# Optimization experiments

Hardware: AMD Instinct MI355X
Metric: run time of the kernel (lower is better)

Reference implementation:

```python
import jax, jax.numpy as jnp
import numpy as np
import math

B, D, S, C, H = 8192, 512, 5, 2048, 4

def setup_inputs() -> dict:
    key = jax.random.key(0)
    ks = jax.random.split(key, 8)
    return {
        "features": jax.random.normal(ks[0], (B, D), dtype=jnp.float32),
        "logits": jax.random.normal(ks[1], (S, B, C), dtype=jnp.float32),
        "scale_feats": jax.random.normal(ks[2], (S, B, D), dtype=jnp.float32),
        "Wq": jax.random.normal(ks[3], (D, D), dtype=jnp.float32) * 0.02,
        "bq": jnp.zeros((D,), jnp.float32),
        "Wk": jax.random.normal(ks[4], (D, D), dtype=jnp.float32) * 0.02,
        "bk": jnp.zeros((D,), jnp.float32),
        "Wv": jax.random.normal(ks[5], (D, D), dtype=jnp.float32) * 0.02,
        "bv": jnp.zeros((D,), jnp.float32),
        "scale_emb": jax.random.normal(ks[6], (S, D), dtype=jnp.float32) * 0.02,
        "temperature": jnp.float32(0.07),
        "attn_w": jnp.ones((3,), jnp.float32) / 3.0,
    }

def reference(features, logits, scale_feats, Wq, bq, Wk, bk, Wv, bv, scale_emb, temperature, attn_w):
    b, d = features.shape
    s = scale_feats.shape[0]
    hd = d // H
    t = jnp.abs(temperature)

    # ---- multihead attention over scales (V is computed in torch but unused) ----
    Q = (features @ Wq + bq).reshape(b, H, hd)                      # [B,H,hd]
    sf_emb = scale_feats + scale_emb[:, None, :]                    # [S,B,D]
    K = (sf_emb @ Wk + bk).reshape(s, b, H, hd)                     # [S,B,H,hd]
    scores = jnp.einsum('bhd,sbhd->bhs', Q, K) / jnp.float32(math.sqrt(hd))
    attn_mha = jax.nn.softmax(scores / t, axis=-1).mean(axis=1)     # [B,S]

    # ---- geometric (angular) attention ----
    fn = features / jnp.linalg.norm(features, axis=-1, keepdims=True).clip(1e-12)
    sfn = scale_feats / jnp.linalg.norm(scale_feats, axis=-1, keepdims=True).clip(1e-12)
    cos_sim = jnp.einsum('bd,sbd->bs', fn, sfn)                     # [B,S]
    angles = jnp.arccos(jnp.clip(cos_sim, -1.0 + 1e-7, 1.0 - 1e-7))
    attn_geo = jax.nn.softmax(jnp.exp(-angles / t), axis=-1)        # [B,S]

    # ---- Cayley-Menger volume-proxy attention ----
    # simplex points: [features, scale_feat, cos(a)*f + sin(a)*s for a in {pi/4, pi/2, 3pi/4}]
    c = jnp.float32(math.sqrt(0.5))
    cf = jnp.array([1.0, 0.0, c, 0.0, -c], jnp.float32)             # coeffs on features
    cs = jnp.array([0.0, 1.0, c, 1.0, c], jnp.float32)              # coeffs on scale_feat
    simplex = (cf[None, :, None, None] * features[None, None] +
               cs[None, :, None, None] * scale_feats[:, None])      # [S,5,B,D]
    norms = jnp.sum(simplex * simplex, axis=-1)                     # [S,5,B]
    gram = jnp.einsum('spbd,sqbd->spqb', simplex, simplex)          # [S,5,5,B]
    distsq = norms[:, :, None] + norms[:, None, :] - 2.0 * gram     # [S,5,5,B]
    volumes = distsq.mean(axis=(1, 2)).T                            # [B,S]
    attn_cay = jax.nn.softmax(volumes / t, axis=-1)

    # ---- fuse attention types ----
    w = jax.nn.softmax(attn_w, axis=0)
    combined = w[0] * attn_mha + w[1] * attn_geo + w[2] * attn_cay  # [B,S]
    combined = combined / combined.sum(axis=-1, keepdims=True)

    combined_logits = jnp.einsum('bs,sbc->bc', combined, logits)    # [B,C]
    return (combined_logits, combined)
```

## Files before the change

kernel.cpp:

```cpp
#include <hip/hip_runtime.h>
#include <math.h>

#define B_N 8192
#define D_N 512
#define S_N 5
#define C_N 2048
#define H_N 4

typedef __attribute__((ext_vector_type(8))) short bf16x8;
typedef __attribute__((ext_vector_type(4))) float floatx4;

__device__ __forceinline__ float bf2f(short u) {
  union { unsigned int i; float f; } c;
  c.i = ((unsigned int)(unsigned short)u) << 16;
  return c.f;
}
__device__ __forceinline__ short f2bf(float f) {
  union { float f; unsigned int i; } c; c.f = f;
  unsigned int x = c.i;
  x += 0x7fffu + ((x >> 16) & 1u);
  return (short)(x >> 16);
}
__device__ __forceinline__ unsigned long long pack4(float a, float b, float c, float d) {
  return (unsigned long long)(unsigned short)f2bf(a)
       | ((unsigned long long)(unsigned short)f2bf(b) << 16)
       | ((unsigned long long)(unsigned short)f2bf(c) << 32)
       | ((unsigned long long)(unsigned short)f2bf(d) << 48);
}

__global__ __launch_bounds__(256) void k_cvt_f(const float* __restrict__ f,
                                               short* __restrict__ fbf, int n8) {
  int i = blockIdx.x * 256 + threadIdx.x;
  if (i >= n8) return;
  const floatx4* p = (const floatx4*)(f + (size_t)i * 8);
  floatx4 a = p[0], b = p[1];
  bf16x8 o;
  o[0] = f2bf(a[0]); o[1] = f2bf(a[1]); o[2] = f2bf(a[2]); o[3] = f2bf(a[3]);
  o[4] = f2bf(b[0]); o[5] = f2bf(b[1]); o[6] = f2bf(b[2]); o[7] = f2bf(b[3]);
  *(bf16x8*)(fbf + (size_t)i * 8) = o;
}

__global__ __launch_bounds__(256) void k_prep(const float* __restrict__ Wq,
                                              const float* __restrict__ Wk,
                                              short* __restrict__ WqT,
                                              short* __restrict__ Wkb) {
  __shared__ float lds[64][65];
  const int bx = blockIdx.x, t = threadIdx.x;
  if (bx < 64) {
    const int r0 = (bx >> 3) * 64, c0 = (bx & 7) * 64;
#pragma unroll
    for (int i = 0; i < 16; ++i) {
      int r = i * 4 + (t >> 6), c = t & 63;
      lds[r][c] = Wq[(size_t)(r0 + r) * 512 + c0 + c];
    }
    __syncthreads();
#pragma unroll
    for (int i = 0; i < 16; ++i) {
      int cL = i * 4 + (t >> 6), rL = t & 63;
      WqT[(size_t)(c0 + cL) * 512 + r0 + rL] = f2bf(lds[rL][cL]);
    }
  } else {
    const int base = (bx - 64) * 8192 + t * 4;
#pragma unroll
    for (int i = 0; i < 8; ++i) {
      int idx = base + i * 1024;
      floatx4 v = *(const floatx4*)(Wk + idx);
      *(unsigned long long*)(Wkb + idx) = pack4(v[0], v[1], v[2], v[3]);
    }
  }
}

__device__ __forceinline__ void gll(const short* g, short* l) {
  __builtin_amdgcn_global_load_lds(
      (const __attribute__((address_space(1))) unsigned int*)(g),
      (__attribute__((address_space(3))) unsigned int*)(l), 16, 0, 0);
}

__global__ __launch_bounds__(256) void k_gemm(
    const short* __restrict__ A, int lda,
    const short* __restrict__ BT, int ldb,
    short* __restrict__ O, int ldo,
    const float* __restrict__ bias, int K, int z_koff, int z_coff) {
  __shared__ __align__(16) short As[2][4096];
  __shared__ __align__(16) short Bs[2][4096];

  const int tid = threadIdx.x;
  const int lane = tid & 63;
  const int wid = tid >> 6;
  const int wr = wid >> 1, wc = wid & 1;
  const int row0 = blockIdx.y * 128;
  const int col0 = blockIdx.x * 128;
  const int z = blockIdx.z;
  const int koff = z * z_koff;
  const int ocoff = z * z_coff;

  const int r1 = tid >> 2, hk = tid & 3;
  const short* Ag1 = A + (size_t)(row0 + r1) * lda + koff + hk * 8;
  const short* Ag2 = A + (size_t)(row0 + 64 + r1) * lda + koff + hk * 8;
  const short* Bg1 = BT + (size_t)(col0 + r1) * ldb + koff + hk * 8;
  const short* Bg2 = BT + (size_t)(col0 + 64 + r1) * ldb + koff + hk * 8;

  floatx4 acc[4][4];
  const floatx4 zero = {0.0f, 0.0f, 0.0f, 0.0f};
#pragma unroll
  for (int m = 0; m < 4; ++m)
#pragma unroll
    for (int n = 0; n < 4; ++n) acc[m][n] = zero;

  const int NT = K >> 5;
  int cur = 0;

  auto stage = [&](int q, int kb) {
    gll(Ag1 + kb, &As[q][tid * 8]);
    gll(Ag2 + kb, &As[q][tid * 8 + 2048]);
    gll(Bg1 + kb, &Bs[q][tid * 8]);
    gll(Bg2 + kb, &Bs[q][tid * 8 + 2048]);
  };

  stage(0, 0);
  __syncthreads();

  for (int t = 0; t < NT; ++t) {
    if (t + 1 < NT) stage(cur ^ 1, (t + 1) * 32);
    bf16x8 af[4], bfr[4];
#pragma unroll
    for (int m = 0; m < 4; ++m)
      af[m] = *(const bf16x8*)&As[cur][(wr * 64 + m * 16 + (lane & 15)) * 32 + (lane >> 4) * 8];
#pragma unroll
    for (int n = 0; n < 4; ++n)
      bfr[n] = *(const bf16x8*)&Bs[cur][(wc * 64 + n * 16 + (lane & 15)) * 32 + (lane >> 4) * 8];
#pragma unroll
    for (int m = 0; m < 4; ++m)
#pragma unroll
      for (int n = 0; n < 4; ++n)
        acc[m][n] = __builtin_amdgcn_mfma_f32_16x16x32_bf16(af[m], bfr[n], acc[m][n], 0, 0, 0);
    __syncthreads();
    cur ^= 1;
  }

#pragma unroll
  for (int m = 0; m < 4; ++m) {
    int rowb = row0 + wr * 64 + m * 16 + (lane >> 4) * 4;
#pragma unroll
    for (int n = 0; n < 4; ++n) {
      int lcol = col0 + wc * 64 + n * 16 + (lane & 15);
      float bv = bias ? bias[lcol] : 0.0f;
      int ocol = ocoff + lcol;
#pragma unroll
      for (int j = 0; j < 4; ++j) {
        O[(size_t)(rowb + j) * ldo + ocol] = f2bf(acc[m][n][j] + bv);
      }
    }
  }
}

__global__ __launch_bounds__(256, 4) void k_fused(
    const float* __restrict__ f, const float* __restrict__ sf,
    const float* __restrict__ emb, const short* __restrict__ Qbf,
    const short* __restrict__ Rbf, const float* __restrict__ bk,
    const float* __restrict__ temp, const float* __restrict__ attn_w,
    const float* __restrict__ logits, float* __restrict__ out,
    float* __restrict__ comb_out) {
  const int lane = threadIdx.x & 63;
  const int wid = threadIdx.x >> 6;
  const int b = blockIdx.x * 4 + wid;
  const int a0 = lane * 8;

  const floatx4* fp = (const floatx4*)(f + (size_t)b * D_N + a0);
  floatx4 fA = fp[0], fB = fp[1];
  float fv[8];
#pragma unroll
  for (int j = 0; j < 4; ++j) { fv[j] = fA[j]; fv[4 + j] = fB[j]; }
  float ffp = 0;
#pragma unroll
  for (int j = 0; j < 8; ++j) ffp += fv[j] * fv[j];

  bf16x8 qv = *(const bf16x8*)(Qbf + (size_t)b * D_N + a0);
  float qbkp = 0;
#pragma unroll
  for (int j = 0; j < 8; ++j) qbkp += bf2f(qv[j]) * bk[a0 + j];

  float rf[H_N][8];
#pragma unroll
  for (int h = 0; h < H_N; ++h) {
    bf16x8 rv = *(const bf16x8*)(Rbf + (size_t)b * 2048 + h * 512 + a0);
#pragma unroll
    for (int j = 0; j < 8; ++j) rf[h][j] = bf2f(rv[j]);
  }

  const int myh = lane >> 4;
  float fs_[S_N], ss_[S_N], sc_[S_N][H_N];

#pragma unroll
  for (int s = 0; s < S_N; ++s) {
    const floatx4* sp = (const floatx4*)(sf + ((size_t)s * B_N + b) * D_N + a0);
    floatx4 sA = sp[0], sB = sp[1];
    const floatx4* ep = (const floatx4*)(emb + (size_t)s * D_N + a0);
    floatx4 eA = ep[0], eB = ep[1];
    float sv[8], se[8];
#pragma unroll
    for (int j = 0; j < 4; ++j) {
      sv[j] = sA[j]; sv[4 + j] = sB[j];
      se[j] = sA[j] + eA[j]; se[4 + j] = sB[j] + eB[j];
    }
    float fsp = 0, ssp = 0;
    float scp[H_N];
#pragma unroll
    for (int h = 0; h < H_N; ++h) scp[h] = (myh == h) ? qbkp : 0.0f;
#pragma unroll
    for (int j = 0; j < 8; ++j) {
      fsp += fv[j] * sv[j];
      ssp += sv[j] * sv[j];
#pragma unroll
      for (int h = 0; h < H_N; ++h) scp[h] += se[j] * rf[h][j];
    }
#pragma unroll
    for (int o = 1; o < 64; o <<= 1) {
      fsp += __shfl_xor(fsp, o, 64);
      ssp += __shfl_xor(ssp, o, 64);
#pragma unroll
      for (int h = 0; h < H_N; ++h) scp[h] += __shfl_xor(scp[h], o, 64);
    }
    fs_[s] = fsp; ss_[s] = ssp;
#pragma unroll
    for (int h = 0; h < H_N; ++h) sc_[s][h] = scp[h];
  }
  float ffv = ffp;
#pragma unroll
  for (int o = 1; o < 64; o <<= 1) ffv += __shfl_xor(ffv, o, 64);

  const float t = fabsf(temp[0]);

  float amha[S_N] = {0, 0, 0, 0, 0};
  const float inv_mha = 1.0f / (sqrtf(128.0f) * t);
#pragma unroll
  for (int h = 0; h < H_N; ++h) {
    float lg[S_N];
#pragma unroll
    for (int s = 0; s < S_N; ++s) lg[s] = sc_[s][h] * inv_mha;
    float mx = lg[0];
#pragma unroll
    for (int s = 1; s < S_N; ++s) mx = fmaxf(mx, lg[s]);
    float e[S_N], sum = 0;
#pragma unroll
    for (int s = 0; s < S_N; ++s) { e[s] = __expf(lg[s] - mx); sum += e[s]; }
    float isum = 0.25f / sum;
#pragma unroll
    for (int s = 0; s < S_N; ++s) amha[s] += e[s] * isum;
  }

  float ageo[S_N];
  {
    const float nf = fmaxf(sqrtf(ffv), 1e-12f);
    float g[S_N];
#pragma unroll
    for (int s = 0; s < S_N; ++s) {
      float ns = fmaxf(sqrtf(ss_[s]), 1e-12f);
      float cs0 = fs_[s] / (nf * ns);
      cs0 = fminf(fmaxf(cs0, -1.0f + 1e-7f), 1.0f - 1e-7f);
      g[s] = __expf(-acosf(cs0) / t);
    }
    float mx = g[0];
#pragma unroll
    for (int s = 1; s < S_N; ++s) mx = fmaxf(mx, g[s]);
    float sum = 0;
#pragma unroll
    for (int s = 0; s < S_N; ++s) { ageo[s] = __expf(g[s] - mx); sum += ageo[s]; }
#pragma unroll
    for (int s = 0; s < S_N; ++s) ageo[s] /= sum;
  }

  float acay[S_N];
  {
    const float SQ2 = 1.41421356237309515f;
    const float Aff = 0.72f;
    const float Ass = 0.72f - 0.32f * SQ2;
    const float Afs = -(8.0f + 4.0f * SQ2) / 25.0f;
    float lg[S_N];
#pragma unroll
    for (int s = 0; s < S_N; ++s)
      lg[s] = (Aff * ffv + Ass * ss_[s] + Afs * fs_[s]) / t;
    float mx = lg[0];
#pragma unroll
    for (int s = 1; s < S_N; ++s) mx = fmaxf(mx, lg[s]);
    float sum = 0;
#pragma unroll
    for (int s = 0; s < S_N; ++s) { acay[s] = __expf(lg[s] - mx); sum += acay[s]; }
#pragma unroll
    for (int s = 0; s < S_N; ++s) acay[s] /= sum;
  }

  float w0 = attn_w[0], w1 = attn_w[1], w2 = attn_w[2];
  float wm = fmaxf(w0, fmaxf(w1, w2));
  float e0 = __expf(w0 - wm), e1 = __expf(w1 - wm), e2 = __expf(w2 - wm);
  float wsum = e0 + e1 + e2;
  w0 = e0 / wsum; w1 = e1 / wsum; w2 = e2 / wsum;

  float cb[S_N], csum = 0;
#pragma unroll
  for (int s = 0; s < S_N; ++s) {
    cb[s] = w0 * amha[s] + w1 * ageo[s] + w2 * acay[s];
    csum += cb[s];
  }
  float ic = 1.0f / csum;
  float cbn[S_N];
#pragma unroll
  for (int s = 0; s < S_N; ++s) cbn[s] = cb[s] * ic;
  if (lane == 0) {
#pragma unroll
    for (int s = 0; s < S_N; ++s) comb_out[(size_t)b * S_N + s] = cbn[s];
  }

  const floatx4 fz = {0.f, 0.f, 0.f, 0.f};
#pragma unroll
  for (int cj = 0; cj < 4; ++cj) {
    const int c0 = cj * 512 + lane * 8;
    floatx4 accA = fz, accB = fz;
#pragma unroll
    for (int s = 0; s < S_N; ++s) {
      const float* lp = logits + ((size_t)s * B_N + b) * C_N + c0;
      floatx4 lA = *(const floatx4*)lp;
      floatx4 lB = *(const floatx4*)(lp + 4);
      accA += lA * cbn[s];
      accB += lB * cbn[s];
    }
    float* op = out + (size_t)b * C_N + c0;
    *(floatx4*)op = accA;
    *(floatx4*)(op + 4) = accB;
  }
}

extern "C" void kernel_launch(void* const* d_in, const int* in_sizes, int n_in,
                              void* d_out, int out_size, void* d_ws, size_t ws_size,
                              hipStream_t stream) {
  const float* features = (const float*)d_in[0];
  const float* logits   = (const float*)d_in[1];
  const float* sf       = (const float*)d_in[2];
  const float* Wq       = (const float*)d_in[3];
  const float* bq       = (const float*)d_in[4];
  const float* Wk       = (const float*)d_in[5];
  const float* bk       = (const float*)d_in[6];
  const float* emb      = (const float*)d_in[9];
  const float* temp     = (const float*)d_in[10];
  const float* attn_w   = (const float*)d_in[11];

  float* out  = (float*)d_out;
  float* comb = out + (size_t)B_N * C_N;

  char* w = (char*)d_ws;
  short* fbf = (short*)(w);
  short* Qbf = (short*)(w + 8388608);
  short* Rbf = (short*)(w + 16777216);
  short* WqT = (short*)(w + 50331648);
  short* Wkb = (short*)(w + 50855936);

  k_cvt_f<<<dim3(2048), dim3(256), 0, stream>>>(features, fbf, 524288);
  k_prep<<<dim3(96), dim3(256), 0, stream>>>(Wq, Wk, WqT, Wkb);
  k_gemm<<<dim3(4, 64, 1), dim3(256), 0, stream>>>(fbf, 512, WqT, 512, Qbf, 512,
                                                   bq, 512, 0, 0);
  k_gemm<<<dim3(4, 64, 4), dim3(256), 0, stream>>>(Qbf, 512, Wkb, 512, Rbf, 2048,
                                                   (const float*)nullptr, 128, 128, 512);
  k_fused<<<dim3(2048), dim3(256), 0, stream>>>(features, sf, emb, Qbf, Rbf, bk,
                                                temp, attn_w, logits, out, comb);
}
```

Before: 159.0 us.

## Precompute per-head Wq·Wk^T products to replace two chained GEMMs with one

Reassociates the score computation so the per-head matrix M_h = Wq_h Wk_h^T is formed once by a small weight-only GEMM, and R = features·M is computed directly in a single K=512 GEMM. Bias terms are folded into precomputed vectors u, v and scalar c. The features conversion and weight preparation are merged into one launch, and the Wq transpose is no longer needed. This removes the intermediate Q GEMM and its round trip through memory. The price is a larger main GEMM (N=2048, K=512 instead of four K=128 slices) and different bf16 rounding, since the weight product is now rounded.

Result: slower. 221.1 us (+39.1%).

```diff
diff --git a/kernel.cpp b/kernel.cpp
--- a/kernel.cpp
+++ b/kernel.cpp
@@ -28,44 +28,67 @@
        | ((unsigned long long)(unsigned short)f2bf(d) << 48);
 }
 
-__global__ __launch_bounds__(256) void k_cvt_f(const float* __restrict__ f,
-                                               short* __restrict__ fbf, int n8) {
-  int i = blockIdx.x * 256 + threadIdx.x;
-  if (i >= n8) return;
-  const floatx4* p = (const floatx4*)(f + (size_t)i * 8);
-  floatx4 a = p[0], b = p[1];
-  bf16x8 o;
-  o[0] = f2bf(a[0]); o[1] = f2bf(a[1]); o[2] = f2bf(a[2]); o[3] = f2bf(a[3]);
-  o[4] = f2bf(b[0]); o[5] = f2bf(b[1]); o[6] = f2bf(b[2]); o[7] = f2bf(b[3]);
-  *(bf16x8*)(fbf + (size_t)i * 8) = o;
-}
-
-__global__ __launch_bounds__(256) void k_prep(const float* __restrict__ Wq,
-                                              const float* __restrict__ Wk,
-                                              short* __restrict__ WqT,
-                                              short* __restrict__ Wkb) {
-  __shared__ float lds[64][65];
+__global__ __launch_bounds__(256) void k_pre(
+    const float* __restrict__ f, const float* __restrict__ Wq,
+    const float* __restrict__ Wk, const float* __restrict__ bq,
+    const float* __restrict__ bk, short* __restrict__ fbf,
+    short* __restrict__ Wqb, short* __restrict__ Wkb,
+    float* __restrict__ u, float* __restrict__ v, float* __restrict__ c) {
   const int bx = blockIdx.x, t = threadIdx.x;
-  if (bx < 64) {
-    const int r0 = (bx >> 3) * 64, c0 = (bx & 7) * 64;
-#pragma unroll
-    for (int i = 0; i < 16; ++i) {
-      int r = i * 4 + (t >> 6), c = t & 63;
-      lds[r][c] = Wq[(size_t)(r0 + r) * 512 + c0 + c];
-    }
-    __syncthreads();
-#pragma unroll
-    for (int i = 0; i < 16; ++i) {
-      int cL = i * 4 + (t >> 6), rL = t & 63;
-      WqT[(size_t)(c0 + cL) * 512 + r0 + rL] = f2bf(lds[rL][cL]);
-    }
-  } else {
-    const int base = (bx - 64) * 8192 + t * 4;
+  if (bx < 2048) {
+    int i = bx * 256 + t;
+    const floatx4* p = (const floatx4*)(f + (size_t)i * 8);
+    floatx4 a = p[0], b = p[1];
+    *(unsigned long long*)(fbf + (size_t)i * 8)     = pack4(a[0], a[1], a[2], a[3]);
+    *(unsigned long long*)(fbf + (size_t)i * 8 + 4) = pack4(b[0], b[1], b[2], b[3]);
+  } else if (bx < 2112) {
+    const float* src = (bx < 2080) ? Wq : Wk;
+    short* dst = (bx < 2080) ? Wqb : Wkb;
+    const int base = ((bx < 2080) ? (bx - 2048) : (bx - 2080)) * 8192 + t * 4;
 #pragma unroll
     for (int i = 0; i < 8; ++i) {
       int idx = base + i * 1024;
-      floatx4 v = *(const floatx4*)(Wk + idx);
-      *(unsigned long long*)(Wkb + idx) = pack4(v[0], v[1], v[2], v[3]);
+      floatx4 w4 = *(const floatx4*)(src + idx);
+      *(unsigned long long*)(dst + idx) = pack4(w4[0], w4[1], w4[2], w4[3]);
+    }
+  } else if (bx == 2112) {
+#pragma unroll
+    for (int i = 0; i < 8; ++i) {
+      int o = i * 256 + t;
+      int h = o >> 9, a = o & 511;
+      const float* wkr = Wk + (size_t)a * 512 + h * 128;
+      const float* bqr = bq + h * 128;
+      float s = 0.0f;
+#pragma unroll 4
+      for (int j = 0; j < 128; j += 4) {
+        floatx4 w4 = *(const floatx4*)(wkr + j);
+        floatx4 b4 = *(const floatx4*)(bqr + j);
+        s += w4[0]*b4[0] + w4[1]*b4[1] + w4[2]*b4[2] + w4[3]*b4[3];
+      }
+      u[o] = s;
+    }
+  } else {
+#pragma unroll
+    for (int i = 0; i < 8; ++i) {
+      int o = i * 256 + t;
+      int d = o >> 2, h = o & 3;
+      const float* wqr = Wq + (size_t)d * 512 + h * 128;
+      const float* bkr = bk + h * 128;
+      float s = 0.0f;
+#pragma unroll 4
+      for (int j = 0; j < 128; j += 4) {
+        floatx4 w4 = *(const floatx4*)(wqr + j);
+        floatx4 b4 = *(const floatx4*)(bkr + j);
+        s += w4[0]*b4[0] + w4[1]*b4[1] + w4[2]*b4[2] + w4[3]*b4[3];
+      }
+      v[o] = s;
+    }
+    if (t < H_N) {
+      const float* bqr = bq + t * 128;
+      const float* bkr = bk + t * 128;
+      float s = 0.0f;
+      for (int j = 0; j < 128; ++j) s += bqr[j] * bkr[j];
+      c[t] = s;
     }
   }
 }
@@ -154,10 +177,86 @@
   }
 }
 
+__global__ __launch_bounds__(256) void k_gemmM(
+    const short* __restrict__ A, int lda,
+    const short* __restrict__ BT, int ldb,
+    short* __restrict__ O, int ldo,
+    int K, int z_koff, int z_coff) {
+  __shared__ __align__(16) short As[2][4096];
+  __shared__ __align__(16) short Bs[2][4096];
+
+  const int tid = threadIdx.x;
+  const int lane = tid & 63;
+  const int wid = tid >> 6;
+  const int wr = wid >> 1, wc = wid & 1;
+  const int row0 = blockIdx.y * 128;
+  const int col0 = blockIdx.x * 128;
+  const int z = blockIdx.z;
+  const int koff = z * z_koff;
+  const int ocoff = z * z_coff;
+
+  const int r1 = tid >> 2, hk = tid & 3;
+  const short* Ag1 = A + (size_t)(row0 + r1) * lda + koff + hk * 8;
+  const short* Ag2 = A + (size_t)(row0 + 64 + r1) * lda + koff + hk * 8;
+  const short* Bg1 = BT + (size_t)(col0 + r1) * ldb + koff + hk * 8;
+  const short* Bg2 = BT + (size_t)(col0 + 64 + r1) * ldb + koff + hk * 8;
+
+  floatx4 acc[4][4];
+  const floatx4 zero = {0.0f, 0.0f, 0.0f, 0.0f};
+#pragma unroll
+  for (int m = 0; m < 4; ++m)
+#pragma unroll
+    for (int n = 0; n < 4; ++n) acc[m][n] = zero;
+
+  const int NT = K >> 5;
+  int cur = 0;
+
+  auto stage = [&](int q, int kb) {
+    gll(Ag1 + kb, &As[q][tid * 8]);
+    gll(Ag2 + kb, &As[q][tid * 8 + 2048]);
+    gll(Bg1 + kb, &Bs[q][tid * 8]);
+    gll(Bg2 + kb, &Bs[q][tid * 8 + 2048]);
+  };
+
+  stage(0, 0);
+  __syncthreads();
+
+  for (int t = 0; t < NT; ++t) {
+    if (t + 1 < NT) stage(cur ^ 1, (t + 1) * 32);
+    bf16x8 af[4], bfr[4];
+#pragma unroll
+    for (int m = 0; m < 4; ++m)
+      af[m] = *(const bf16x8*)&As[cur][(wr * 64 + m * 16 + (lane & 15)) * 32 + (lane >> 4) * 8];
+#pragma unroll
+    for (int n = 0; n < 4; ++n)
+      bfr[n] = *(const bf16x8*)&Bs[cur][(wc * 64 + n * 16 + (lane & 15)) * 32 + (lane >> 4) * 8];
+#pragma unroll
+    for (int m = 0; m < 4; ++m)
+#pragma unroll
+      for (int n = 0; n < 4; ++n)
+        acc[m][n] = __builtin_amdgcn_mfma_f32_16x16x32_bf16(af[m], bfr[n], acc[m][n], 0, 0, 0);
+    __syncthreads();
+    cur ^= 1;
+  }
+
+#pragma unroll
+  for (int m = 0; m < 4; ++m) {
+    int rowb = row0 + wr * 64 + m * 16 + (lane >> 4) * 4;
+#pragma unroll
+    for (int n = 0; n < 4; ++n) {
+      int ocol = ocoff + col0 + wc * 64 + n * 16 + (lane & 15);
+#pragma unroll
+      for (int j = 0; j < 4; ++j) {
+        O[(size_t)ocol * ldo + rowb + j] = f2bf(acc[m][n][j]);
+      }
+    }
+  }
+}
+
 __global__ __launch_bounds__(256, 4) void k_fused(
     const float* __restrict__ f, const float* __restrict__ sf,
-    const float* __restrict__ emb, const short* __restrict__ Qbf,
-    const short* __restrict__ Rbf, const float* __restrict__ bk,
+    const float* __restrict__ emb, const short* __restrict__ Rbf,
+    const float* __restrict__ vbuf, const float* __restrict__ cbuf,
     const float* __restrict__ temp, const float* __restrict__ attn_w,
     const float* __restrict__ logits, float* __restrict__ out,
     float* __restrict__ comb_out) {
@@ -175,10 +274,20 @@
 #pragma unroll
   for (int j = 0; j < 8; ++j) ffp += fv[j] * fv[j];
 
-  bf16x8 qv = *(const bf16x8*)(Qbf + (size_t)b * D_N + a0);
-  float qbkp = 0;
-#pragma unroll
-  for (int j = 0; j < 8; ++j) qbkp += bf2f(qv[j]) * bk[a0 + j];
+  float cinit[H_N];
+  {
+    float qbk[H_N] = {0, 0, 0, 0};
+    const floatx4* vp = (const floatx4*)(vbuf + (size_t)a0 * 4);
+#pragma unroll
+    for (int j = 0; j < 8; ++j) {
+      floatx4 vv = vp[j];
+#pragma unroll
+      for (int h = 0; h < H_N; ++h) qbk[h] += fv[j] * vv[h];
+    }
+#pragma unroll
+    for (int h = 0; h < H_N; ++h)
+      cinit[h] = qbk[h] + (lane == 0 ? cbuf[h] : 0.0f);
+  }
 
   float rf[H_N][8];
 #pragma unroll
@@ -188,7 +297,6 @@
     for (int j = 0; j < 8; ++j) rf[h][j] = bf2f(rv[j]);
   }
 
-  const int myh = lane >> 4;
   float fs_[S_N], ss_[S_N], sc_[S_N][H_N];
 
 #pragma unroll
@@ -206,7 +314,7 @@
     float fsp = 0, ssp = 0;
     float scp[H_N];
 #pragma unroll
-    for (int h = 0; h < H_N; ++h) scp[h] = (myh == h) ? qbkp : 0.0f;
+    for (int h = 0; h < H_N; ++h) scp[h] = cinit[h];
 #pragma unroll
     for (int j = 0; j < 8; ++j) {
       fsp += fv[j] * sv[j];
@@ -228,6 +336,7 @@
   float ffv = ffp;
 #pragma unroll
   for (int o = 1; o < 64; o <<= 1) ffv += __shfl_xor(ffv, o, 64);
+
 
   const float t = fabsf(temp[0]);
 
@@ -349,17 +458,20 @@
 
   char* w = (char*)d_ws;
   short* fbf = (short*)(w);
-  short* Qbf = (short*)(w + 8388608);
+  short* Wqb = (short*)(w + 8388608);
+  short* Wkb = (short*)(w + 8912896);
+  short* MT  = (short*)(w + 9437184);
+  float* ub  = (float*)(w + 11534336);
+  float* vb  = (float*)(w + 11542528);
+  float* cb  = (float*)(w + 11550720);
   short* Rbf = (short*)(w + 16777216);
-  short* WqT = (short*)(w + 50331648);
-  short* Wkb = (short*)(w + 50855936);
-
-  k_cvt_f<<<dim3(2048), dim3(256), 0, stream>>>(features, fbf, 524288);
-  k_prep<<<dim3(96), dim3(256), 0, stream>>>(Wq, Wk, WqT, Wkb);
-  k_gemm<<<dim3(4, 64, 1), dim3(256), 0, stream>>>(fbf, 512, WqT, 512, Qbf, 512,
-                                                   bq, 512, 0, 0);
-  k_gemm<<<dim3(4, 64, 4), dim3(256), 0, stream>>>(Qbf, 512, Wkb, 512, Rbf, 2048,
-                                                   (const float*)nullptr, 128, 128, 512);
-  k_fused<<<dim3(2048), dim3(256), 0, stream>>>(features, sf, emb, Qbf, Rbf, bk,
+
+  k_pre<<<dim3(2114), dim3(256), 0, stream>>>(features, Wq, Wk, bq, bk,
+                                              fbf, Wqb, Wkb, ub, vb, cb);
+  k_gemmM<<<dim3(4, 4, 4), dim3(256), 0, stream>>>(Wqb, 512, Wkb, 512, MT, 512,
+                                                   128, 128, 512);
+  k_gemm<<<dim3(16, 64, 1), dim3(256), 0, stream>>>(fbf, 512, MT, 512, Rbf, 2048,
+                                                    ub, 512, 0, 0);
+  k_fused<<<dim3(2048), dim3(256), 0, stream>>>(features, sf, emb, Rbf, vb, cb,
                                                 temp, attn_w, logits, out, comb);
 }
```
